# Kernel optimization log

Measured on AMD Instinct MI355X. Metric: run time of the kernel, lower is better.

The kernel has to match this reference:

```python
import jax, jax.numpy as jnp
import numpy as np

N, E, R = 100000, 1600000, 64
DIN, DREL, DOUT, H = 32, 32, 64, 8
DH = DOUT // H


def setup_inputs() -> dict:
    key = jax.random.key(0)
    ks = jax.random.split(key, 10)
    emb_ent = jax.random.normal(ks[0], (N, DIN), dtype=jnp.float32)
    emb_rel = jax.random.normal(ks[1], (R, DREL), dtype=jnp.float32)
    attn_W = jax.random.normal(ks[2], (DOUT, 2 * DIN + DREL), dtype=jnp.float32) * 0.1
    attn_b = jnp.zeros((DOUT,), dtype=jnp.float32)
    attn_vec = jax.random.normal(ks[3], (1, H, DH), dtype=jnp.float32) * 0.1
    aggr_W = jax.random.normal(ks[4], (DOUT, DIN + DREL), dtype=jnp.float32) * 0.1
    aggr_b = jnp.zeros((DOUT,), dtype=jnp.float32)
    head_idxs = jax.random.randint(ks[5], (E,), 0, N, dtype=jnp.int32)
    # guarantee every node has at least one incoming edge (well-formed graph)
    tail_idxs = jnp.concatenate([
        jnp.arange(N, dtype=jnp.int32),
        jax.random.randint(ks[6], (E - N,), 0, N, dtype=jnp.int32),
    ])
    rel_idxs = jax.random.randint(ks[7], (E,), 0, R, dtype=jnp.int32)
    return {"emb_ent": emb_ent, "emb_rel": emb_rel, "attn_W": attn_W,
            "attn_b": attn_b, "attn_vec": attn_vec, "aggr_W": aggr_W,
            "aggr_b": aggr_b, "head_idxs": head_idxs, "tail_idxs": tail_idxs,
            "rel_idxs": rel_idxs}


def reference(emb_ent, emb_rel, attn_W, attn_b, attn_vec, aggr_W, aggr_b,
              head_idxs, tail_idxs, rel_idxs):
    num_ent = emb_ent.shape[0]
    # mean incoming relation embedding per entity (self-loop relation)
    edge_rel = emb_rel[rel_idxs]                                   # [E, Drel]
    ent_freq = jax.ops.segment_sum(jnp.ones_like(tail_idxs, dtype=edge_rel.dtype),
                                   tail_idxs, num_segments=num_ent)[:, None]
    self_rel = jax.ops.segment_sum(edge_rel, tail_idxs, num_segments=num_ent) / ent_freq
    # append self-loops
    emb_rels = jnp.concatenate([edge_rel, self_rel], axis=0)       # [E+N, Drel]
    loop = jnp.arange(num_ent, dtype=head_idxs.dtype)
    head = jnp.concatenate([head_idxs, loop])                      # [E+N]
    tail = jnp.concatenate([tail_idxs, loop])                      # [E+N]
    ent_tail = emb_ent[tail]
    ent_head = emb_ent[head]
    # attention logits per edge per head
    cat_att = jnp.concatenate([ent_tail, ent_head, emb_rels], axis=-1)  # [E+N, 2*Din+Drel]
    proj = jax.nn.leaky_relu(cat_att @ attn_W.T + attn_b, negative_slope=0.2)
    proj = proj.reshape(-1, H, DH)
    attn_raw = jnp.sum(proj * attn_vec, axis=-1, keepdims=True)    # [E+N, H, 1]
    # segment-softmax over incoming edges of each tail node
    amax = jax.ops.segment_max(attn_raw, tail, num_segments=num_ent)
    attn_val = jnp.exp(attn_raw - amax[tail])
    attn_sum = jax.ops.segment_sum(attn_val, tail, num_segments=num_ent)
    beta = attn_val / (attn_sum[tail] + 1e-16)                     # [E+N, H, 1]
    # weighted message aggregation
    cat_msg = jnp.concatenate([ent_head, emb_rels], axis=-1)       # [E+N, Din+Drel]
    msg = (cat_msg @ aggr_W.T + aggr_b).reshape(-1, H, DH)
    out = jax.ops.segment_sum(beta * msg, tail, num_segments=num_ent)  # [N, H, DH]
    return out.reshape(num_ent, H * DH)
```

## Files before the change

### kernel.cpp

```cpp
#include <hip/hip_runtime.h>
#include <math.h>

#define DIN 32
#define DREL 32
#define CATA 96
#define CATM 64
#define LOG2E 1.44269504088896340736f
#define MAXD 64

#define SCAT_B 2048
#define ART_B 16
#define ENT_B 512

__device__ __forceinline__ ushort f2bf(float x) {
  unsigned u = __float_as_uint(x);
  return (ushort)((u + 0x7FFFu + ((u >> 16) & 1u)) >> 16);
}
__device__ __forceinline__ float bfhi(unsigned v) { return __uint_as_float(v & 0xFFFF0000u); }
__device__ __forceinline__ float bflo(unsigned v) { return __uint_as_float(v << 16); }

__device__ __forceinline__ float fexp2(float x) {
#if __has_builtin(__builtin_amdgcn_exp2f)
  return __builtin_amdgcn_exp2f(x);
#else
  return __expf(x * 0.6931471805599453f);
#endif
}

__global__ __launch_bounds__(256) void k1_kernel(
    const float* __restrict__ emb_ent, const float* __restrict__ emb_rel,
    const float* __restrict__ attn_W, const float* __restrict__ aggr_W,
    const int* __restrict__ head_idxs, const int* __restrict__ tail_idxs,
    const int* __restrict__ rel_idxs,
    int* __restrict__ cnt, int* __restrict__ emeta, float2* __restrict__ ART,
    ushort* __restrict__ A_tail, unsigned* __restrict__ entT2,
    int N, int R, int E) {
  int b = blockIdx.x;
  if (b < SCAT_B) {
    int tid = b * 256 + threadIdx.x;
    for (int e = tid; e < E; e += SCAT_B * 256) {
      int t = tail_idxs[e];
      int slot = atomicAdd(&cnt[t], 1);
      if (slot < MAXD)
        emeta[((size_t)t << 6) + slot] = (head_idxs[e] << 8) | rel_idxs[e];
    }
  } else if (b < SCAT_B + ART_B) {
    int i = (b - SCAT_B) * 256 + threadIdx.x;
    if (i < R * 64) {
      int r = i >> 6, o = i & 63;
      const float* er = emb_rel + r * DREL;
      float a = 0.f, t = 0.f;
#pragma unroll
      for (int k = 0; k < DREL; ++k) {
        float e = er[k];
        a = fmaf(attn_W[o * CATA + 2 * DIN + k], e, a);
        t = fmaf(aggr_W[o * CATM + DIN + k], e, t);
      }
      ART[i] = make_float2(a, t);
    }
  } else {
    int rb = b - SCAT_B - ART_B;
    int role = rb / ENT_B;
    int eb = rb - role * ENT_B;
    int lane = threadIdx.x & 63;
    int wid = __builtin_amdgcn_readfirstlane((int)((eb * 256 + threadIdx.x) >> 6));
    const int NW = ENT_B * 4;
    const float* wsrc = (role == 0) ? (attn_W + lane * CATA)
                      : (role == 1) ? (attn_W + lane * CATA + DIN)
                                    : (aggr_W + lane * CATM);
    float w[DIN];
#pragma unroll
    for (int k = 0; k < DIN; ++k) w[k] = wsrc[k];
    ushort* entH = (ushort*)entT2;
    for (int n = wid; n < N; n += NW) {
      const float* ent = emb_ent + (size_t)n * DIN;
      float d = 0.f;
#pragma unroll
      for (int k = 0; k < DIN; ++k) d = fmaf(w[k], ent[k], d);
      ushort bf = f2bf(d);
      size_t idx = ((size_t)n << 6) + lane;
      if (role == 0)      A_tail[idx] = bf;
      else if (role == 1) entH[2 * idx + 1] = bf;
      else                entH[2 * idx + 0] = bf;
    }
  }
}

__global__ __launch_bounds__(256) void node_agg_kernel(
    const ushort* __restrict__ A_tail, const unsigned* __restrict__ entT2,
    const float2* __restrict__ ART,
    const float* __restrict__ attn_b, const float* __restrict__ attn_vec,
    const float* __restrict__ aggr_b,
    const int* __restrict__ emeta, const int* __restrict__ cnt,
    float* __restrict__ out, int N, int totalWaves) {
  int wid = __builtin_amdgcn_readfirstlane((int)((blockIdx.x * blockDim.x + threadIdx.x) >> 6));
  int lane = threadIdx.x & 63;
  float avec = attn_vec[lane] * LOG2E;
  float ab = attn_b[lane];
  float gb = aggr_b[lane];

  for (int t = wid; t < N; t += totalWaves) {
    int len = cnt[t];
    if (len > MAXD) len = MAXD;
    const int* ebase = emeta + ((size_t)t << 6);
    float at = __uint_as_float(((unsigned)A_tail[((size_t)t << 6) + lane]) << 16) + ab;
    float m0 = -INFINITY, s0 = 0.f, a0 = 0.f;
    float m1 = -INFINITY, s1 = 0.f, a1 = 0.f;
    float suma = 0.f, sumt = 0.f;
    for (int base = 0; base < len; base += 64) {
      int nch = len - base; if (nch > 64) nch = 64;
      int sel = lane < nch ? lane : nch - 1;
      int mload = ebase[base + sel];
      int i = 0;
      for (; i + 2 <= nch; i += 2) {
        int mmA = __builtin_amdgcn_readlane(mload, i);
        int mmB = __builtin_amdgcn_readlane(mload, i + 1);
        int hnA = mmA >> 8, rA = mmA & 255;
        int hnB = mmB >> 8, rB = mmB & 255;
        unsigned pvA = entT2[((size_t)hnA << 6) + lane];
        float2 rtA = ART[(rA << 6) + lane];
        unsigned pvB = entT2[((size_t)hnB << 6) + lane];
        float2 rtB = ART[(rB << 6) + lane];
        suma += rtA.x + rtB.x;
        sumt += rtA.y + rtB.y;
        float preA = at + bfhi(pvA) + rtA.x;
        float vA = fmaxf(preA, 0.2f * preA) * avec;
        vA += __shfl_xor(vA, 1); vA += __shfl_xor(vA, 2); vA += __shfl_xor(vA, 4);
        float preB = at + bfhi(pvB) + rtB.x;
        float vB = fmaxf(preB, 0.2f * preB) * avec;
        vB += __shfl_xor(vB, 1); vB += __shfl_xor(vB, 2); vB += __shfl_xor(vB, 4);
        float mn0 = fmaxf(m0, vA);
        float c0 = fexp2(m0 - mn0), e0 = fexp2(vA - mn0);
        s0 = fmaf(s0, c0, e0);
        a0 = fmaf(a0, c0, e0 * (bflo(pvA) + rtA.y));
        m0 = mn0;
        float mn1 = fmaxf(m1, vB);
        float c1 = fexp2(m1 - mn1), e1 = fexp2(vB - mn1);
        s1 = fmaf(s1, c1, e1);
        a1 = fmaf(a1, c1, e1 * (bflo(pvB) + rtB.y));
        m1 = mn1;
      }
      if (i < nch) {
        int mm = __builtin_amdgcn_readlane(mload, i);
        int hn = mm >> 8, r = mm & 255;
        unsigned pv = entT2[((size_t)hn << 6) + lane];
        float2 rt = ART[(r << 6) + lane];
        suma += rt.x;
        sumt += rt.y;
        float pre = at + bfhi(pv) + rt.x;
        float v = fmaxf(pre, 0.2f * pre) * avec;
        v += __shfl_xor(v, 1); v += __shfl_xor(v, 2); v += __shfl_xor(v, 4);
        float mn0 = fmaxf(m0, v);
        float c0 = fexp2(m0 - mn0), e0 = fexp2(v - mn0);
        s0 = fmaf(s0, c0, e0);
        a0 = fmaf(a0, c0, e0 * (bflo(pv) + rt.y));
        m0 = mn0;
      }
    }
    float m = fmaxf(m0, m1);
    float c0 = fexp2(m0 - m), c1 = fexp2(m1 - m);
    float s = fmaf(s0, c0, s1 * c1);
    float acc = fmaf(a0, c0, a1 * c1);
    float invd = 1.f / (float)len;
    unsigned pv = entT2[((size_t)t << 6) + lane];
    float pre = at + bfhi(pv) + suma * invd;
    float v = fmaxf(pre, 0.2f * pre) * avec;
    v += __shfl_xor(v, 1); v += __shfl_xor(v, 2); v += __shfl_xor(v, 4);
    float mn = fmaxf(m, v);
    float c = fexp2(m - mn);
    float e = fexp2(v - mn);
    s = fmaf(s, c, e);
    acc = fmaf(acc, c, e * (bflo(pv) + sumt * invd));
    out[((size_t)t << 6) + lane] = acc / (s + 1e-16f) + gb;
  }
}

extern "C" void kernel_launch(void* const* d_in, const int* in_sizes, int n_in,
                              void* d_out, int out_size, void* d_ws, size_t ws_size,
                              hipStream_t stream) {
  const float* emb_ent  = (const float*)d_in[0];
  const float* emb_rel  = (const float*)d_in[1];
  const float* attn_W   = (const float*)d_in[2];
  const float* attn_b   = (const float*)d_in[3];
  const float* attn_vec = (const float*)d_in[4];
  const float* aggr_W   = (const float*)d_in[5];
  const float* aggr_b   = (const float*)d_in[6];
  const int* head_idxs  = (const int*)d_in[7];
  const int* tail_idxs  = (const int*)d_in[8];
  const int* rel_idxs   = (const int*)d_in[9];

  const int N = in_sizes[0] / DIN;
  const int R = in_sizes[1] / DREL;
  const int E = in_sizes[7];
  float* out = (float*)d_out;

  char* ws = (char*)d_ws;
  size_t off = 0;
  int* cnt   = (int*)(ws + off); off += (size_t)N * sizeof(int);
  int* emeta = (int*)(ws + off); off += (size_t)N * MAXD * sizeof(int);
  ushort* A_tail  = (ushort*)(ws + off);   off += (size_t)N * 64 * sizeof(ushort);
  unsigned* entT2 = (unsigned*)(ws + off); off += (size_t)N * 64 * sizeof(unsigned);
  float2* ART = (float2*)(ws + off); off += (size_t)R * 64 * sizeof(float2);

  hipMemsetAsync(cnt, 0, (size_t)N * sizeof(int), stream);

  k1_kernel<<<SCAT_B + ART_B + 3 * ENT_B, 256, 0, stream>>>(
      emb_ent, emb_rel, attn_W, aggr_W, head_idxs, tail_idxs, rel_idxs,
      cnt, emeta, ART, A_tail, entT2, N, R, E);
  const int NB = 2048;
  node_agg_kernel<<<NB, 256, 0, stream>>>(A_tail, entT2, ART, attn_b, attn_vec, aggr_b,
                                          emeta, cnt, out, N, NB * 4);
}
```

Measured before the change: 360.9 us.

## Split interleaved head tables and pad per-node edge counters to 64 bytes

```diff
diff --git a/kernel.cpp b/kernel.cpp
--- a/kernel.cpp
+++ b/kernel.cpp
@@ -16,8 +16,9 @@
   unsigned u = __float_as_uint(x);
   return (ushort)((u + 0x7FFFu + ((u >> 16) & 1u)) >> 16);
 }
-__device__ __forceinline__ float bfhi(unsigned v) { return __uint_as_float(v & 0xFFFF0000u); }
-__device__ __forceinline__ float bflo(unsigned v) { return __uint_as_float(v << 16); }
+__device__ __forceinline__ float bf2f(ushort x) {
+  return __uint_as_float(((unsigned)x) << 16);
+}
 
 __device__ __forceinline__ float fexp2(float x) {
 #if __has_builtin(__builtin_amdgcn_exp2f)
@@ -32,15 +33,15 @@
     const float* __restrict__ attn_W, const float* __restrict__ aggr_W,
     const int* __restrict__ head_idxs, const int* __restrict__ tail_idxs,
     const int* __restrict__ rel_idxs,
-    int* __restrict__ cnt, int* __restrict__ emeta, float2* __restrict__ ART,
-    ushort* __restrict__ A_tail, unsigned* __restrict__ entT2,
+    int* __restrict__ cnt16, int* __restrict__ emeta, float2* __restrict__ ART,
+    ushort* __restrict__ A_tail, ushort* __restrict__ A_head, ushort* __restrict__ M_ent,
     int N, int R, int E) {
   int b = blockIdx.x;
   if (b < SCAT_B) {
     int tid = b * 256 + threadIdx.x;
     for (int e = tid; e < E; e += SCAT_B * 256) {
       int t = tail_idxs[e];
-      int slot = atomicAdd(&cnt[t], 1);
+      int slot = atomicAdd(&cnt16[t << 4], 1);
       if (slot < MAXD)
         emeta[((size_t)t << 6) + slot] = (head_idxs[e] << 8) | rel_idxs[e];
     }
@@ -68,30 +69,26 @@
     const float* wsrc = (role == 0) ? (attn_W + lane * CATA)
                       : (role == 1) ? (attn_W + lane * CATA + DIN)
                                     : (aggr_W + lane * CATM);
+    ushort* dst = (role == 0) ? A_tail : (role == 1) ? A_head : M_ent;
     float w[DIN];
 #pragma unroll
     for (int k = 0; k < DIN; ++k) w[k] = wsrc[k];
-    ushort* entH = (ushort*)entT2;
     for (int n = wid; n < N; n += NW) {
       const float* ent = emb_ent + (size_t)n * DIN;
       float d = 0.f;
 #pragma unroll
       for (int k = 0; k < DIN; ++k) d = fmaf(w[k], ent[k], d);
-      ushort bf = f2bf(d);
-      size_t idx = ((size_t)n << 6) + lane;
-      if (role == 0)      A_tail[idx] = bf;
-      else if (role == 1) entH[2 * idx + 1] = bf;
-      else                entH[2 * idx + 0] = bf;
+      dst[((size_t)n << 6) + lane] = f2bf(d);
     }
   }
 }
 
 __global__ __launch_bounds__(256) void node_agg_kernel(
-    const ushort* __restrict__ A_tail, const unsigned* __restrict__ entT2,
-    const float2* __restrict__ ART,
+    const ushort* __restrict__ A_tail, const ushort* __restrict__ A_head,
+    const ushort* __restrict__ M_ent, const float2* __restrict__ ART,
     const float* __restrict__ attn_b, const float* __restrict__ attn_vec,
     const float* __restrict__ aggr_b,
-    const int* __restrict__ emeta, const int* __restrict__ cnt,
+    const int* __restrict__ emeta, const int* __restrict__ cnt16,
     float* __restrict__ out, int N, int totalWaves) {
   int wid = __builtin_amdgcn_readfirstlane((int)((blockIdx.x * blockDim.x + threadIdx.x) >> 6));
   int lane = threadIdx.x & 63;
@@ -100,10 +97,10 @@
   float gb = aggr_b[lane];
 
   for (int t = wid; t < N; t += totalWaves) {
-    int len = cnt[t];
+    int len = cnt16[t << 4];
     if (len > MAXD) len = MAXD;
     const int* ebase = emeta + ((size_t)t << 6);
-    float at = __uint_as_float(((unsigned)A_tail[((size_t)t << 6) + lane]) << 16) + ab;
+    float at = bf2f(A_tail[((size_t)t << 6) + lane]) + ab;
     float m0 = -INFINITY, s0 = 0.f, a0 = 0.f;
     float m1 = -INFINITY, s1 = 0.f, a1 = 0.f;
     float suma = 0.f, sumt = 0.f;
@@ -117,43 +114,46 @@
         int mmB = __builtin_amdgcn_readlane(mload, i + 1);
         int hnA = mmA >> 8, rA = mmA & 255;
         int hnB = mmB >> 8, rB = mmB & 255;
-        unsigned pvA = entT2[((size_t)hnA << 6) + lane];
+        float ahA = bf2f(A_head[((size_t)hnA << 6) + lane]);
+        float meA = bf2f(M_ent[((size_t)hnA << 6) + lane]);
         float2 rtA = ART[(rA << 6) + lane];
-        unsigned pvB = entT2[((size_t)hnB << 6) + lane];
+        float ahB = bf2f(A_head[((size_t)hnB << 6) + lane]);
+        float meB = bf2f(M_ent[((size_t)hnB << 6) + lane]);
         float2 rtB = ART[(rB << 6) + lane];
         suma += rtA.x + rtB.x;
         sumt += rtA.y + rtB.y;
-        float preA = at + bfhi(pvA) + rtA.x;
+        float preA = at + ahA + rtA.x;
         float vA = fmaxf(preA, 0.2f * preA) * avec;
         vA += __shfl_xor(vA, 1); vA += __shfl_xor(vA, 2); vA += __shfl_xor(vA, 4);
-        float preB = at + bfhi(pvB) + rtB.x;
+        float preB = at + ahB + rtB.x;
         float vB = fmaxf(preB, 0.2f * preB) * avec;
         vB += __shfl_xor(vB, 1); vB += __shfl_xor(vB, 2); vB += __shfl_xor(vB, 4);
         float mn0 = fmaxf(m0, vA);
         float c0 = fexp2(m0 - mn0), e0 = fexp2(vA - mn0);
         s0 = fmaf(s0, c0, e0);
-        a0 = fmaf(a0, c0, e0 * (bflo(pvA) + rtA.y));
+        a0 = fmaf(a0, c0, e0 * (meA + rtA.y));
         m0 = mn0;
         float mn1 = fmaxf(m1, vB);
         float c1 = fexp2(m1 - mn1), e1 = fexp2(vB - mn1);
         s1 = fmaf(s1, c1, e1);
-        a1 = fmaf(a1, c1, e1 * (bflo(pvB) + rtB.y));
+        a1 = fmaf(a1, c1, e1 * (meB + rtB.y));
         m1 = mn1;
       }
       if (i < nch) {
         int mm = __builtin_amdgcn_readlane(mload, i);
         int hn = mm >> 8, r = mm & 255;
-        unsigned pv = entT2[((size_t)hn << 6) + lane];
+        float ah = bf2f(A_head[((size_t)hn << 6) + lane]);
+        float me = bf2f(M_ent[((size_t)hn << 6) + lane]);
         float2 rt = ART[(r << 6) + lane];
         suma += rt.x;
         sumt += rt.y;
-        float pre = at + bfhi(pv) + rt.x;
+        float pre = at + ah + rt.x;
         float v = fmaxf(pre, 0.2f * pre) * avec;
         v += __shfl_xor(v, 1); v += __shfl_xor(v, 2); v += __shfl_xor(v, 4);
         float mn0 = fmaxf(m0, v);
         float c0 = fexp2(m0 - mn0), e0 = fexp2(v - mn0);
         s0 = fmaf(s0, c0, e0);
-        a0 = fmaf(a0, c0, e0 * (bflo(pv) + rt.y));
+        a0 = fmaf(a0, c0, e0 * (me + rt.y));
         m0 = mn0;
       }
     }
@@ -162,15 +162,16 @@
     float s = fmaf(s0, c0, s1 * c1);
     float acc = fmaf(a0, c0, a1 * c1);
     float invd = 1.f / (float)len;
-    unsigned pv = entT2[((size_t)t << 6) + lane];
-    float pre = at + bfhi(pv) + suma * invd;
+    float ah = bf2f(A_head[((size_t)t << 6) + lane]);
+    float me = bf2f(M_ent[((size_t)t << 6) + lane]);
+    float pre = at + ah + suma * invd;
     float v = fmaxf(pre, 0.2f * pre) * avec;
     v += __shfl_xor(v, 1); v += __shfl_xor(v, 2); v += __shfl_xor(v, 4);
     float mn = fmaxf(m, v);
     float c = fexp2(m - mn);
     float e = fexp2(v - mn);
     s = fmaf(s, c, e);
-    acc = fmaf(acc, c, e * (bflo(pv) + sumt * invd));
+    acc = fmaf(acc, c, e * (me + sumt * invd));
     out[((size_t)t << 6) + lane] = acc / (s + 1e-16f) + gb;
   }
 }
@@ -196,18 +197,20 @@
 
   char* ws = (char*)d_ws;
   size_t off = 0;
-  int* cnt   = (int*)(ws + off); off += (size_t)N * sizeof(int);
+  int* cnt16 = (int*)(ws + off); off += (size_t)N * 16 * sizeof(int);
   int* emeta = (int*)(ws + off); off += (size_t)N * MAXD * sizeof(int);
-  ushort* A_tail  = (ushort*)(ws + off);   off += (size_t)N * 64 * sizeof(ushort);
-  unsigned* entT2 = (unsigned*)(ws + off); off += (size_t)N * 64 * sizeof(unsigned);
+  ushort* A_tail = (ushort*)(ws + off); off += (size_t)N * 64 * sizeof(ushort);
+  ushort* A_head = (ushort*)(ws + off); off += (size_t)N * 64 * sizeof(ushort);
+  ushort* M_ent  = (ushort*)(ws + off); off += (size_t)N * 64 * sizeof(ushort);
   float2* ART = (float2*)(ws + off); off += (size_t)R * 64 * sizeof(float2);
 
-  hipMemsetAsync(cnt, 0, (size_t)N * sizeof(int), stream);
+  hipMemsetAsync(cnt16, 0, (size_t)N * 16 * sizeof(int), stream);
 
   k1_kernel<<<SCAT_B + ART_B + 3 * ENT_B, 256, 0, stream>>>(
       emb_ent, emb_rel, attn_W, aggr_W, head_idxs, tail_idxs, rel_idxs,
-      cnt, emeta, ART, A_tail, entT2, N, R, E);
+      cnt16, emeta, ART, A_tail, A_head, M_ent, N, R, E);
   const int NB = 2048;
-  node_agg_kernel<<<NB, 256, 0, stream>>>(A_tail, entT2, ART, attn_b, attn_vec, aggr_b,
-                                          emeta, cnt, out, N, NB * 4);
-}
+  node_agg_kernel<<<NB, 256, 0, stream>>>(A_tail, A_head, M_ent, ART,
+                                          attn_b, attn_vec, aggr_b,
+                                          emeta, cnt16, out, N, NB * 4);
+}
```

After: 331.8 us. -8.1%, faster.
